# Performance work log

Measured on AMD Instinct MI355X. Metric: run time of the kernel, lower is better.

The kernel has to match this reference:

```python
import jax, jax.numpy as jnp
import numpy as np

N = 100000   # nodes
E = 600000   # edges
C = 128      # feature dim
LN_EPS = 1e-5


def setup_inputs() -> dict:
    key = jax.random.key(0)
    k = jax.random.split(key, 5)
    h = jax.random.normal(k[0], (N, C), dtype=jnp.float32)
    edge_index = jax.random.randint(k[1], (2, E), 0, N)
    edge_weight = jax.random.uniform(k[2], (E,), dtype=jnp.float32)
    W = jax.random.normal(k[3], (C, C), dtype=jnp.float32) / np.sqrt(C).astype(np.float32)
    b = jax.random.normal(k[4], (C,), dtype=jnp.float32) * 0.01
    gamma = jnp.ones((C,), jnp.float32)
    beta = jnp.zeros((C,), jnp.float32)
    return {"h": h, "edge_index": edge_index, "edge_weight": edge_weight,
            "W": W, "b": b, "gamma": gamma, "beta": beta}


def reference(h, edge_index, edge_weight, W, b, gamma, beta):
    n = h.shape[0]
    self_idx = jnp.arange(n)
    # add self-loops with weight 1
    src = jnp.concatenate([edge_index[0], self_idx])
    dst = jnp.concatenate([edge_index[1], self_idx])
    ew = jnp.concatenate([edge_weight, jnp.ones((n,), h.dtype)])
    # symmetric normalization: deg over dst, d = deg^{-1/2} clamped at 1e4
    deg = jax.ops.segment_sum(ew, dst, num_segments=n)
    d = jnp.minimum(deg ** -0.5, 10000.0)
    norm = d[src] * ew * d[dst]                      # [E+N]
    msg = h[src] * norm[:, None]                     # [E+N, C]
    agg = jax.ops.segment_sum(msg, dst, num_segments=n)  # [N, C]
    # linear + residual + layernorm + exact GELU (dropout = identity in eval)
    x = agg @ W.T + b + h
    mean = jnp.mean(x, axis=-1, keepdims=True)
    var = jnp.mean(jnp.square(x - mean), axis=-1, keepdims=True)
    y = gamma * (x - mean) * jax.lax.rsqrt(var + LN_EPS) + beta
    return jax.nn.gelu(y, approximate=False)
```

## Files before the change

kernel.cpp:

```cpp
#include <hip/hip_runtime.h>

constexpr int C = 128;
#define SCAN_CHUNK 1024

typedef __attribute__((ext_vector_type(8))) short short8;
typedef __attribute__((ext_vector_type(4))) float f32x4;

__device__ __forceinline__ unsigned short f2bf(float f) {
  unsigned int u = __float_as_uint(f);
  unsigned int r = (u + 0x7fffu + ((u >> 16) & 1u)) >> 16;
  return (unsigned short)r;
}
__device__ __forceinline__ float bfl(unsigned int p) { return __uint_as_float(p << 16); }
__device__ __forceinline__ float bfh(unsigned int p) { return __uint_as_float(p & 0xffff0000u); }

template <int DO_HB>
__global__ void k_prep_all(const float* __restrict__ W, unsigned short* __restrict__ Wb,
                           const float* __restrict__ h, unsigned short* __restrict__ hb,
                           int total4, unsigned long long* __restrict__ packed, int n) {
  const int stride = gridDim.x * blockDim.x;
  const int gid = blockIdx.x * blockDim.x + threadIdx.x;
  for (int i = gid; i < C * C / 4; i += stride) {
    float4 w = ((const float4*)W)[i];
    uint2 pk;
    pk.x = f2bf(w.x) | ((unsigned int)f2bf(w.y) << 16);
    pk.y = f2bf(w.z) | ((unsigned int)f2bf(w.w) << 16);
    ((uint2*)Wb)[i] = pk;
  }
  if (DO_HB) {
    for (int i = gid; i < total4; i += stride) {
      float4 w = ((const float4*)h)[i];
      uint2 pk;
      pk.x = f2bf(w.x) | ((unsigned int)f2bf(w.y) << 16);
      pk.y = f2bf(w.z) | ((unsigned int)f2bf(w.w) << 16);
      ((uint2*)hb)[i] = pk;
    }
  }
  for (int i = gid; i < n; i += stride) packed[i] = 0ull;
}

__global__ void k_edge_deg(const int* __restrict__ dst, const float* __restrict__ ew,
                           unsigned long long* __restrict__ packed,
                           int* __restrict__ slot, int e) {
  int i = blockIdx.x * blockDim.x + threadIdx.x;
  if (i < e) {
    unsigned long long enc =
        (1ull << 40) | (unsigned long long)(ew[i] * 4294967296.0f);
    unsigned long long old = atomicAdd(&packed[dst[i]], enc);
    slot[i] = (int)(old >> 40);
  }
}

__global__ void k_scan1(const unsigned long long* __restrict__ packed,
                        float* __restrict__ d, int* __restrict__ excl,
                        int* __restrict__ sums, int n) {
  __shared__ int l[256];
  const int t = threadIdx.x;
  const int base = blockIdx.x * SCAN_CHUNK + t * 4;
  int v0 = 0, v1 = 0, v2 = 0, v3 = 0;
  const float fs = 1.0f / 4294967296.0f;
  const unsigned long long M = (1ull << 40) - 1ull;
  if (base + 0 < n) { unsigned long long p = packed[base + 0]; v0 = (int)(p >> 40);
    d[base + 0] = fminf(1.0f / sqrtf(1.0f + (float)(p & M) * fs), 10000.0f); }
  if (base + 1 < n) { unsigned long long p = packed[base + 1]; v1 = (int)(p >> 40);
    d[base + 1] = fminf(1.0f / sqrtf(1.0f + (float)(p & M) * fs), 10000.0f); }
  if (base + 2 < n) { unsigned long long p = packed[base + 2]; v2 = (int)(p >> 40);
    d[base + 2] = fminf(1.0f / sqrtf(1.0f + (float)(p & M) * fs), 10000.0f); }
  if (base + 3 < n) { unsigned long long p = packed[base + 3]; v3 = (int)(p >> 40);
    d[base + 3] = fminf(1.0f / sqrtf(1.0f + (float)(p & M) * fs), 10000.0f); }
  const int s = v0 + v1 + v2 + v3;
  l[t] = s; __syncthreads();
  for (int off = 1; off < 256; off <<= 1) {
    int x = 0;
    if (t >= off) x = l[t - off];
    __syncthreads();
    l[t] += x;
    __syncthreads();
  }
  int ex = l[t] - s;
  if (t == 255) sums[blockIdx.x] = l[t];
  if (base + 0 < n) excl[base + 0] = ex;  ex += v0;
  if (base + 1 < n) excl[base + 1] = ex;  ex += v1;
  if (base + 2 < n) excl[base + 2] = ex;  ex += v2;
  if (base + 3 < n) excl[base + 3] = ex;
}

__global__ void k_scan2(int* __restrict__ sums, int nb) {
  __shared__ int l[256];
  const int t = threadIdx.x;
  const int s = (t < nb) ? sums[t] : 0;
  l[t] = s; __syncthreads();
  for (int off = 1; off < 256; off <<= 1) {
    int x = 0;
    if (t >= off) x = l[t - off];
    __syncthreads();
    l[t] += x;
    __syncthreads();
  }
  if (t < nb) sums[t] = l[t] - s;
}

__global__ void k_scan3(int* __restrict__ rowptr, const int* __restrict__ sums,
                        int n, int e) {
  int i = blockIdx.x * blockDim.x + threadIdx.x;
  if (i < n) rowptr[i] += sums[i >> 10];
  if (i == 0) rowptr[n] = e;
}

__global__ void k_scatter(const int* __restrict__ src, const int* __restrict__ dst,
                          const float* __restrict__ ew, const float* __restrict__ d,
                          const int* __restrict__ rowptr, const int* __restrict__ slot,
                          int2* __restrict__ meta, int e) {
  int i = blockIdx.x * blockDim.x + threadIdx.x;
  if (i < e) {
    int t = dst[i], s = src[i];
    float nm = d[s] * ew[i] * d[t];
    int p = rowptr[t] + slot[i];
    meta[p] = make_int2(s, __float_as_int(nm));
  }
}

template <int USE_HB, int OUT_BF>
__global__ void k_gather(const int* __restrict__ rowptr, const int2* __restrict__ meta,
                         const float* __restrict__ d, const float* __restrict__ h,
                         const unsigned short* __restrict__ hb,
                         float* __restrict__ aggf, unsigned short* __restrict__ aggb,
                         int n) {
  int g = blockIdx.x * blockDim.x + threadIdx.x;
  int v = g >> 5, lane = g & 31;
  if (v >= n) return;
  const int cb = lane * 4;
  const float dv = d[v];
  const float dd = dv * dv;
  float4 acc;
  if (USE_HB) {
    uint2 hv = *(const uint2*)(hb + (size_t)v * C + cb);
    acc = make_float4(bfl(hv.x) * dd, bfh(hv.x) * dd, bfl(hv.y) * dd, bfh(hv.y) * dd);
  } else {
    float4 hv = *(const float4*)(h + (size_t)v * C + cb);
    acc = make_float4(hv.x * dd, hv.y * dd, hv.z * dd, hv.w * dd);
  }
  int p = rowptr[v];
  const int end = rowptr[v + 1];
  if (USE_HB) {
    for (; p + 4 <= end; p += 4) {
      int2 m0 = meta[p], m1 = meta[p + 1], m2 = meta[p + 2], m3 = meta[p + 3];
      float n0 = __int_as_float(m0.y), n1 = __int_as_float(m1.y);
      float n2 = __int_as_float(m2.y), n3 = __int_as_float(m3.y);
      uint2 x0 = *(const uint2*)(hb + (size_t)m0.x * C + cb);
      uint2 x1 = *(const uint2*)(hb + (size_t)m1.x * C + cb);
      uint2 x2 = *(const uint2*)(hb + (size_t)m2.x * C + cb);
      uint2 x3 = *(const uint2*)(hb + (size_t)m3.x * C + cb);
      acc.x += bfl(x0.x) * n0 + bfl(x1.x) * n1 + bfl(x2.x) * n2 + bfl(x3.x) * n3;
      acc.y += bfh(x0.x) * n0 + bfh(x1.x) * n1 + bfh(x2.x) * n2 + bfh(x3.x) * n3;
      acc.z += bfl(x0.y) * n0 + bfl(x1.y) * n1 + bfl(x2.y) * n2 + bfl(x3.y) * n3;
      acc.w += bfh(x0.y) * n0 + bfh(x1.y) * n1 + bfh(x2.y) * n2 + bfh(x3.y) * n3;
    }
    for (; p < end; ++p) {
      int2 m0 = meta[p];
      float n0 = __int_as_float(m0.y);
      uint2 x0 = *(const uint2*)(hb + (size_t)m0.x * C + cb);
      acc.x += bfl(x0.x) * n0; acc.y += bfh(x0.x) * n0;
      acc.z += bfl(x0.y) * n0; acc.w += bfh(x0.y) * n0;
    }
  } else {
    for (; p + 4 <= end; p += 4) {
      int2 m0 = meta[p], m1 = meta[p + 1], m2 = meta[p + 2], m3 = meta[p + 3];
      float n0 = __int_as_float(m0.y), n1 = __int_as_float(m1.y);
      float n2 = __int_as_float(m2.y), n3 = __int_as_float(m3.y);
      float4 x0 = *(const float4*)(h + (size_t)m0.x * C + cb);
      float4 x1 = *(const float4*)(h + (size_t)m1.x * C + cb);
      float4 x2 = *(const float4*)(h + (size_t)m2.x * C + cb);
      float4 x3 = *(const float4*)(h + (size_t)m3.x * C + cb);
      acc.x += x0.x * n0 + x1.x * n1 + x2.x * n2 + x3.x * n3;
      acc.y += x0.y * n0 + x1.y * n1 + x2.y * n2 + x3.y * n3;
      acc.z += x0.z * n0 + x1.z * n1 + x2.z * n2 + x3.z * n3;
      acc.w += x0.w * n0 + x1.w * n1 + x2.w * n2 + x3.w * n3;
    }
    for (; p < end; ++p) {
      int2 m0 = meta[p];
      float n0 = __int_as_float(m0.y);
      float4 x0 = *(const float4*)(h + (size_t)m0.x * C + cb);
      acc.x += x0.x * n0; acc.y += x0.y * n0; acc.z += x0.z * n0; acc.w += x0.w * n0;
    }
  }
  if (OUT_BF) {
    uint2 pk;
    pk.x = f2bf(acc.x) | ((unsigned int)f2bf(acc.y) << 16);
    pk.y = f2bf(acc.z) | ((unsigned int)f2bf(acc.w) << 16);
    *(uint2*)(aggb + (size_t)v * C + cb) = pk;
  } else {
    *(float4*)(aggf + (size_t)v * C + cb) = acc;
  }
}

#define TM 64

template <int IN_BF>
__launch_bounds__(256, 3)
__global__ void k_mfma_ln_gelu(const float* __restrict__ aggf,
                               const unsigned short* __restrict__ aggb,
                               const float* __restrict__ h,
                               const unsigned short* __restrict__ Wb,
                               const float* __restrict__ b,
                               const float* __restrict__ gamma, const float* __restrict__ beta,
                               float* __restrict__ out, int n) {
  __shared__ char lds[48 * 1024];
  char* Wl = lds;
  char* Al = lds + 32768;
  const int tid = threadIdx.x;
  const int row0 = blockIdx.x * TM;

  #pragma unroll
  for (int i = 0; i < 8; ++i) {
    int u = tid + i * 256;
    int j = u >> 4, un = u & 15;
    uint4 w = ((const uint4*)Wb)[u];
    *(uint4*)(Wl + j * 256 + ((un * 16) ^ ((j & 7) << 4))) = w;
  }
  #pragma unroll
  for (int i = 0; i < 8; ++i) {
    int u = tid + i * 256;
    int j = u >> 5;
    int rr = row0 + j; if (rr >= n) rr = n - 1;
    uint2 pk;
    if (IN_BF) {
      pk = ((const uint2*)(aggb + (size_t)rr * C))[u & 31];
    } else {
      float4 a = ((const float4*)(aggf + (size_t)rr * C))[u & 31];
      pk.x = f2bf(a.x) | ((unsigned int)f2bf(a.y) << 16);
      pk.y = f2bf(a.z) | ((unsigned int)f2bf(a.w) << 16);
    }
    *(uint2*)(Al + j * 256 + (((u & 31) * 8) ^ ((j & 7) << 4))) = pk;
  }
  __syncthreads();

  const int lane = tid & 63;
  const int wt   = tid >> 6;
  const int c16  = lane & 15;
  const int quad = lane >> 4;

  f32x4 acc[8];
  #pragma unroll
  for (int jt = 0; jt < 8; ++jt) acc[jt] = (f32x4){0.f, 0.f, 0.f, 0.f};

  const int abase = (wt * 16 + c16) * 256;
  const int swz   = (c16 & 7) << 4;
  #pragma unroll
  for (int ks = 0; ks < 4; ++ks) {
    const int koff = ks * 64 + quad * 16;
    short8 af = *(const short8*)(Al + abase + (koff ^ swz));
    #pragma unroll
    for (int jt = 0; jt < 8; ++jt) {
      short8 bf = *(const short8*)(Wl + (jt * 16 + c16) * 256 + (koff ^ swz));
      acc[jt] = __builtin_amdgcn_mfma_f32_16x16x32_bf16(af, bf, acc[jt], 0, 0, 0);
    }
  }

  float bj[8], gj[8], btj[8];
  #pragma unroll
  for (int jt = 0; jt < 8; ++jt) {
    int j = jt * 16 + c16;
    bj[jt] = b[j]; gj[jt] = gamma[j]; btj[jt] = beta[j];
  }

  #pragma unroll
  for (int i = 0; i < 4; ++i) {
    const int row = row0 + wt * 16 + quad * 4 + i;
    const bool ok = row < n;
    const float* hrow = h + (size_t)row * C;
    float x[8];
    float s = 0.f, t2 = 0.f;
    #pragma unroll
    for (int jt = 0; jt < 8; ++jt) {
      float v = acc[jt][i] + bj[jt] + (ok ? hrow[jt * 16 + c16] : 0.f);
      x[jt] = v; s += v; t2 += v * v;
    }
    #pragma unroll
    for (int m = 8; m >= 1; m >>= 1) {
      s += __shfl_xor(s, m, 16); t2 += __shfl_xor(t2, m, 16);
    }
    const float inv = 1.0f / C;
    float mean = s * inv;
    float var  = t2 * inv - mean * mean;
    float rstd = rsqrtf(var + 1e-5f);
    if (ok) {
      float* orow = out + (size_t)row * C;
      #pragma unroll
      for (int jt = 0; jt < 8; ++jt) {
        float y = gj[jt] * ((x[jt] - mean) * rstd) + btj[jt];
        orow[jt * 16 + c16] = 0.5f * y * (1.0f + erff(y * 0.70710678118f));
      }
    }
  }
}

extern "C" void kernel_launch(void* const* d_in, const int* in_sizes, int n_in,
                              void* d_out, int out_size, void* d_ws, size_t ws_size,
                              hipStream_t stream) {
  const float* h     = (const float*)d_in[0];
  const int*   ei    = (const int*)d_in[1];
  const float* ew    = (const float*)d_in[2];
  const float* W     = (const float*)d_in[3];
  const float* b     = (const float*)d_in[4];
  const float* gamma = (const float*)d_in[5];
  const float* beta  = (const float*)d_in[6];

  const int n = in_sizes[0] / C;
  const int e = in_sizes[2];
  const int* src = ei;
  const int* dst = ei + e;

  float* out = (float*)d_out;

  int2* meta    = (int2*)d_ws;
  unsigned long long* packed = (unsigned long long*)(meta + e);
  int* slot     = (int*)(packed + n);
  float* d      = (float*)(slot + e);
  int* rowptr   = (int*)(d + n);
  int* sums     = rowptr + (n + 1);
  unsigned short* Wb = (unsigned short*)(sums + 256);
  unsigned short* hb = Wb + C * C;
  unsigned short* aggb = hb + (size_t)n * C;

  const size_t need_mid  = (size_t)((char*)(hb + (size_t)n * C) - (char*)d_ws);
  const size_t need_full = (size_t)((char*)(aggb + (size_t)n * C) - (char*)d_ws);
  const int mode = (ws_size >= need_full) ? 2 : (ws_size >= need_mid) ? 1 : 0;

  const int nb = (n + SCAN_CHUNK - 1) / SCAN_CHUNK;
  const int total4 = n * C / 4;

  if (mode >= 1)
    k_prep_all<1><<<1024, 256, 0, stream>>>(W, Wb, h, hb, total4, packed, n);
  else
    k_prep_all<0><<<1024, 256, 0, stream>>>(W, Wb, h, hb, total4, packed, n);

  k_edge_deg<<<(e + 255) / 256, 256, 0, stream>>>(dst, ew, packed, slot, e);
  k_scan1   <<<nb, 256, 0, stream>>>(packed, d, rowptr, sums, n);
  k_scan2   <<<1, 256, 0, stream>>>(sums, nb);
  k_scan3   <<<(n + 255) / 256, 256, 0, stream>>>(rowptr, sums, n, e);
  k_scatter <<<(e + 255) / 256, 256, 0, stream>>>(src, dst, ew, d, rowptr, slot, meta, e);

  const long gthreads = (long)n * 32;
  const int ggrid = (int)((gthreads + 255) / 256);
  const int mgrid = (n + TM - 1) / TM;

  if (mode == 2) {
    k_gather<1, 1><<<ggrid, 256, 0, stream>>>(rowptr, meta, d, h, hb, out, aggb, n);
    k_mfma_ln_gelu<1><<<mgrid, 256, 0, stream>>>(out, aggb, h, Wb, b, gamma, beta, out, n);
  } else if (mode == 1) {
    k_gather<1, 0><<<ggrid, 256, 0, stream>>>(rowptr, meta, d, h, hb, out, aggb, n);
    k_mfma_ln_gelu<0><<<mgrid, 256, 0, stream>>>(out, aggb, h, Wb, b, gamma, beta, out, n);
  } else {
    k_gather<0, 0><<<ggrid, 256, 0, stream>>>(rowptr, meta, d, h, hb, out, aggb, n);
    k_mfma_ln_gelu<0><<<mgrid, 256, 0, stream>>>(out, aggb, h, Wb, b, gamma, beta, out, n);
  }
}
```

Baseline: 138.8 us.

## Fuse scan kernels, read bf16 residual, use nontemporal loads and stores

```diff
diff --git a/kernel.cpp b/kernel.cpp
--- a/kernel.cpp
+++ b/kernel.cpp
@@ -5,6 +5,8 @@
 
 typedef __attribute__((ext_vector_type(8))) short short8;
 typedef __attribute__((ext_vector_type(4))) float f32x4;
+typedef __attribute__((ext_vector_type(2))) unsigned int u32x2;
+typedef __attribute__((ext_vector_type(4))) unsigned int u32x4;
 
 __device__ __forceinline__ unsigned short f2bf(float f) {
   unsigned int u = __float_as_uint(f);
@@ -29,11 +31,11 @@
   }
   if (DO_HB) {
     for (int i = gid; i < total4; i += stride) {
-      float4 w = ((const float4*)h)[i];
-      uint2 pk;
+      f32x4 w = __builtin_nontemporal_load(&((const f32x4*)h)[i]);
+      u32x2 pk;
       pk.x = f2bf(w.x) | ((unsigned int)f2bf(w.y) << 16);
       pk.y = f2bf(w.z) | ((unsigned int)f2bf(w.w) << 16);
-      ((uint2*)hb)[i] = pk;
+      ((u32x2*)hb)[i] = pk;
     }
   }
   for (int i = gid; i < n; i += stride) packed[i] = 0ull;
@@ -85,8 +87,10 @@
   if (base + 3 < n) excl[base + 3] = ex;
 }
 
-__global__ void k_scan2(int* __restrict__ sums, int nb) {
+__global__ void k_scan23(int* __restrict__ rowptr, const int* __restrict__ sums,
+                         int nb, int n, int e) {
   __shared__ int l[256];
+  __shared__ int pre[256];
   const int t = threadIdx.x;
   const int s = (t < nb) ? sums[t] : 0;
   l[t] = s; __syncthreads();
@@ -97,14 +101,11 @@
     l[t] += x;
     __syncthreads();
   }
-  if (t < nb) sums[t] = l[t] - s;
-}
-
-__global__ void k_scan3(int* __restrict__ rowptr, const int* __restrict__ sums,
-                        int n, int e) {
-  int i = blockIdx.x * blockDim.x + threadIdx.x;
-  if (i < n) rowptr[i] += sums[i >> 10];
-  if (i == 0) rowptr[n] = e;
+  pre[t] = l[t] - s;
+  __syncthreads();
+  const int i = blockIdx.x * 256 + t;
+  if (i < n) rowptr[i] += pre[i >> 10];
+  else if (i == n) rowptr[n] = e;
 }
 
 __global__ void k_scatter(const int* __restrict__ src, const int* __restrict__ dst,
@@ -132,6 +133,7 @@
   const int cb = lane * 4;
   const float dv = d[v];
   const float dd = dv * dv;
+  const u32x2* mp = (const u32x2*)meta;
   float4 acc;
   if (USE_HB) {
     uint2 hv = *(const uint2*)(hb + (size_t)v * C + cb);
@@ -144,9 +146,12 @@
   const int end = rowptr[v + 1];
   if (USE_HB) {
     for (; p + 4 <= end; p += 4) {
-      int2 m0 = meta[p], m1 = meta[p + 1], m2 = meta[p + 2], m3 = meta[p + 3];
-      float n0 = __int_as_float(m0.y), n1 = __int_as_float(m1.y);
-      float n2 = __int_as_float(m2.y), n3 = __int_as_float(m3.y);
+      u32x2 m0 = __builtin_nontemporal_load(mp + p);
+      u32x2 m1 = __builtin_nontemporal_load(mp + p + 1);
+      u32x2 m2 = __builtin_nontemporal_load(mp + p + 2);
+      u32x2 m3 = __builtin_nontemporal_load(mp + p + 3);
+      float n0 = __uint_as_float(m0.y), n1 = __uint_as_float(m1.y);
+      float n2 = __uint_as_float(m2.y), n3 = __uint_as_float(m3.y);
       uint2 x0 = *(const uint2*)(hb + (size_t)m0.x * C + cb);
       uint2 x1 = *(const uint2*)(hb + (size_t)m1.x * C + cb);
       uint2 x2 = *(const uint2*)(hb + (size_t)m2.x * C + cb);
@@ -157,17 +162,20 @@
       acc.w += bfh(x0.y) * n0 + bfh(x1.y) * n1 + bfh(x2.y) * n2 + bfh(x3.y) * n3;
     }
     for (; p < end; ++p) {
-      int2 m0 = meta[p];
-      float n0 = __int_as_float(m0.y);
+      u32x2 m0 = __builtin_nontemporal_load(mp + p);
+      float n0 = __uint_as_float(m0.y);
       uint2 x0 = *(const uint2*)(hb + (size_t)m0.x * C + cb);
       acc.x += bfl(x0.x) * n0; acc.y += bfh(x0.x) * n0;
       acc.z += bfl(x0.y) * n0; acc.w += bfh(x0.y) * n0;
     }
   } else {
     for (; p + 4 <= end; p += 4) {
-      int2 m0 = meta[p], m1 = meta[p + 1], m2 = meta[p + 2], m3 = meta[p + 3];
-      float n0 = __int_as_float(m0.y), n1 = __int_as_float(m1.y);
-      float n2 = __int_as_float(m2.y), n3 = __int_as_float(m3.y);
+      u32x2 m0 = __builtin_nontemporal_load(mp + p);
+      u32x2 m1 = __builtin_nontemporal_load(mp + p + 1);
+      u32x2 m2 = __builtin_nontemporal_load(mp + p + 2);
+      u32x2 m3 = __builtin_nontemporal_load(mp + p + 3);
+      float n0 = __uint_as_float(m0.y), n1 = __uint_as_float(m1.y);
+      float n2 = __uint_as_float(m2.y), n3 = __uint_as_float(m3.y);
       float4 x0 = *(const float4*)(h + (size_t)m0.x * C + cb);
       float4 x1 = *(const float4*)(h + (size_t)m1.x * C + cb);
       float4 x2 = *(const float4*)(h + (size_t)m2.x * C + cb);
@@ -178,17 +186,17 @@
       acc.w += x0.w * n0 + x1.w * n1 + x2.w * n2 + x3.w * n3;
     }
     for (; p < end; ++p) {
-      int2 m0 = meta[p];
-      float n0 = __int_as_float(m0.y);
+      u32x2 m0 = __builtin_nontemporal_load(mp + p);
+      float n0 = __uint_as_float(m0.y);
       float4 x0 = *(const float4*)(h + (size_t)m0.x * C + cb);
       acc.x += x0.x * n0; acc.y += x0.y * n0; acc.z += x0.z * n0; acc.w += x0.w * n0;
     }
   }
   if (OUT_BF) {
-    uint2 pk;
+    u32x2 pk;
     pk.x = f2bf(acc.x) | ((unsigned int)f2bf(acc.y) << 16);
     pk.y = f2bf(acc.z) | ((unsigned int)f2bf(acc.w) << 16);
-    *(uint2*)(aggb + (size_t)v * C + cb) = pk;
+    __builtin_nontemporal_store(pk, (u32x2*)(aggb + (size_t)v * C + cb));
   } else {
     *(float4*)(aggf + (size_t)v * C + cb) = acc;
   }
@@ -196,11 +204,12 @@
 
 #define TM 64
 
-template <int IN_BF>
+template <int IN_BF, int RES_BF>
 __launch_bounds__(256, 3)
 __global__ void k_mfma_ln_gelu(const float* __restrict__ aggf,
                                const unsigned short* __restrict__ aggb,
                                const float* __restrict__ h,
+                               const unsigned short* __restrict__ hb,
                                const unsigned short* __restrict__ Wb,
                                const float* __restrict__ b,
                                const float* __restrict__ gamma, const float* __restrict__ beta,
@@ -268,12 +277,20 @@
   for (int i = 0; i < 4; ++i) {
     const int row = row0 + wt * 16 + quad * 4 + i;
     const bool ok = row < n;
-    const float* hrow = h + (size_t)row * C;
     float x[8];
     float s = 0.f, t2 = 0.f;
     #pragma unroll
     for (int jt = 0; jt < 8; ++jt) {
-      float v = acc[jt][i] + bj[jt] + (ok ? hrow[jt * 16 + c16] : 0.f);
+      float res = 0.f;
+      if (ok) {
+        if (RES_BF) {
+          unsigned short rh = hb[(size_t)row * C + jt * 16 + c16];
+          res = __uint_as_float((unsigned int)rh << 16);
+        } else {
+          res = h[(size_t)row * C + jt * 16 + c16];
+        }
+      }
+      float v = acc[jt][i] + bj[jt] + res;
       x[jt] = v; s += v; t2 += v * v;
     }
     #pragma unroll
@@ -289,7 +306,8 @@
       #pragma unroll
       for (int jt = 0; jt < 8; ++jt) {
         float y = gj[jt] * ((x[jt] - mean) * rstd) + btj[jt];
-        orow[jt * 16 + c16] = 0.5f * y * (1.0f + erff(y * 0.70710678118f));
+        float g = 0.5f * y * (1.0f + erff(y * 0.70710678118f));
+        __builtin_nontemporal_store(g, &orow[jt * 16 + c16]);
       }
     }
   }
@@ -337,8 +355,7 @@
 
   k_edge_deg<<<(e + 255) / 256, 256, 0, stream>>>(dst, ew, packed, slot, e);
   k_scan1   <<<nb, 256, 0, stream>>>(packed, d, rowptr, sums, n);
-  k_scan2   <<<1, 256, 0, stream>>>(sums, nb);
-  k_scan3   <<<(n + 255) / 256, 256, 0, stream>>>(rowptr, sums, n, e);
+  k_scan23  <<<(n + 256) / 256, 256, 0, stream>>>(rowptr, sums, nb, n, e);
   k_scatter <<<(e + 255) / 256, 256, 0, stream>>>(src, dst, ew, d, rowptr, slot, meta, e);
 
   const long gthreads = (long)n * 32;
@@ -347,12 +364,12 @@
 
   if (mode == 2) {
     k_gather<1, 1><<<ggrid, 256, 0, stream>>>(rowptr, meta, d, h, hb, out, aggb, n);
-    k_mfma_ln_gelu<1><<<mgrid, 256, 0, stream>>>(out, aggb, h, Wb, b, gamma, beta, out, n);
+    k_mfma_ln_gelu<1, 1><<<mgrid, 256, 0, stream>>>(out, aggb, h, hb, Wb, b, gamma, beta, out, n);
   } else if (mode == 1) {
     k_gather<1, 0><<<ggrid, 256, 0, stream>>>(rowptr, meta, d, h, hb, out, aggb, n);
-    k_mfma_ln_gelu<0><<<mgrid, 256, 0, stream>>>(out, aggb, h, Wb, b, gamma, beta, out, n);
+    k_mfma_ln_gelu<0, 1><<<mgrid, 256, 0, stream>>>(out, aggb, h, hb, Wb, b, gamma, beta, out, n);
   } else {
     k_gather<0, 0><<<ggrid, 256, 0, stream>>>(rowptr, meta, d, h, hb, out, aggb, n);
-    k_mfma_ln_gelu<0><<<mgrid, 256, 0, stream>>>(out, aggb, h, Wb, b, gamma, beta, out, n);
-  }
-}
+    k_mfma_ln_gelu<0, 0><<<mgrid, 256, 0, stream>>>(out, aggb, h, hb, Wb, b, gamma, beta, out, n);
+  }
+}
```

New measurement: 157.1 us. +13.2%, slower.
